# Kernel tuning notes

Measured on AMD Instinct MI355X. Metric: run time of the kernel, lower is better.

The kernel has to match this reference:

```python
import jax, jax.numpy as jnp
import numpy as np

N = 100_000      # lidar points (KITTI-scale)
E = 800_000      # knn edges, avg degree 8
C_IN = 4
INTERNAL_H, INTERNAL_W = 240, 1216   # INTERNAL_IMG_SIZE


def setup_inputs() -> dict:
    key = jax.random.key(0)
    ks = jax.random.split(key, 16)
    x = jax.random.normal(ks[0], (N, C_IN), jnp.float32)
    # lidar-like points in velodyne frame: x fwd [5,70], y left [-20,20], z up [-2,1]
    u = jax.random.uniform(ks[1], (N, 3), jnp.float32)
    pos = jnp.stack([5.0 + 65.0 * u[:, 0],
                     -20.0 + 40.0 * u[:, 1],
                     -2.0 + 3.0 * u[:, 2]], axis=1)
    edge_index = jax.random.randint(ks[2], (2, E), 0, N, dtype=jnp.int32)
    batch = jnp.zeros((N,), jnp.int32)
    # folded calibration P2 @ R0 @ Tr: pinhole cam looking down velodyne +x
    f, cx, cy = 720.0, 621.0, 250.0
    proj = jnp.array([[cx, -f, 0.0, 0.0],
                      [cy, 0.0, -f, 0.0],
                      [1.0, 0.0, 0.0, 0.0]], jnp.float32)
    dims = [(C_IN + 3, 64), (64 + 3, 128), (128 + 3, 256)]
    params = {}
    ki = 3
    for li, (din, dout) in enumerate(dims, 1):
        s1, s2 = 1.0 / np.sqrt(din), 1.0 / np.sqrt(dout)
        params[f"w1_{li}"] = jax.random.uniform(ks[ki], (din, dout), jnp.float32, -s1, s1); ki += 1
        params[f"b1_{li}"] = jnp.zeros((dout,), jnp.float32)
        params[f"w2_{li}"] = jax.random.uniform(ks[ki], (dout, dout), jnp.float32, -s2, s2); ki += 1
        params[f"b2_{li}"] = jnp.zeros((dout,), jnp.float32)
    return dict(x=x, pos=pos, edge_index=edge_index, batch=batch, proj=proj,
                img_h=375, img_w=1242, **params)


def _pointnet_conv(x, pos, src, dst, w1, b1, w2, b2):
    # message: local_nn([x_j, pos_j - pos_i]) with MLP = lin1 -> relu -> lin2; aggr = max
    m = jnp.concatenate([x[src], pos[src] - pos[dst]], axis=1)     # [E', din]
    h = jnp.maximum(m @ w1 + b1, 0.0) @ w2 + b2                    # [E', dout]
    return jax.ops.segment_max(h, dst, num_segments=x.shape[0])


def reference(x, pos, edge_index, batch, proj, img_h, img_w,
              w1_1, b1_1, w2_1, b2_1,
              w1_2, b1_2, w2_2, b2_2,
              w1_3, b1_3, w2_3, b2_3):
    n = x.shape[0]
    # PointNetConv adds self-loops by default -> every segment non-empty
    loops = jnp.arange(n, dtype=edge_index.dtype)
    src = jnp.concatenate([edge_index[0], loops])
    dst = jnp.concatenate([edge_index[1], loops])

    h = _pointnet_conv(x, pos, src, dst, w1_1, b1_1, w2_1, b2_1)   # [N, 64]
    h = _pointnet_conv(h, pos, src, dst, w1_2, b1_2, w2_2, b2_2)   # [N, 128]
    h = _pointnet_conv(h, pos, src, dst, w1_3, b1_3, w2_3, b2_3)   # [N, 256]

    # projection: (proj @ [pos; 1]) -> [3, N]; perspective divide; int16 trunc
    hom = proj @ jnp.concatenate([pos.T, jnp.ones((1, n), pos.dtype)], axis=0)
    off_u, off_v = img_w - INTERNAL_W, img_h - INTERNAL_H
    ui = (hom[0] / hom[2]).astype(jnp.int16).astype(jnp.int32) - off_u
    vi = (hom[1] / hom[2]).astype(jnp.int16).astype(jnp.int32) - off_v
    valid = (ui >= 0) & (vi >= 0) & (ui < INTERNAL_W) & (vi < INTERNAL_H)
    # route invalid points out-of-bounds so mode='drop' discards them
    ui = jnp.where(valid, ui, INTERNAL_W)
    vi = jnp.where(valid, vi, INTERNAL_H)

    img = jnp.zeros((1, h.shape[1], INTERNAL_W, INTERNAL_H), h.dtype)  # (B=1, C, 1216, 240)
    img = img.at[0, :, ui, vi].add(h, mode='drop')

    # max_pool2d(kernel=4, stride=4) -> (1, 256, 304, 60)
    B, C, W, H = img.shape
    pooled = img.reshape(B, C, W // 4, 4, H // 4, 4).max(axis=(3, 5))
    return pooled
```

## Files before the change

kernel.cpp:

```cpp
#include <hip/hip_runtime.h>
#include <cstdint>

#define N_PTS 100000
#define N_EDGE 800000
#define N_ITEMS (N_EDGE + N_PTS)
#define IMG_W 1216
#define IMG_H 240
#define OW 304
#define OH 60
#define CHUNK 32
#define BIN_BLOCKS 391

typedef _Float16 f16;
typedef _Float16 f16x8 __attribute__((ext_vector_type(8)));
typedef float f32x4 __attribute__((ext_vector_type(4)));

__device__ __forceinline__ void atomicMaxF(float* addr, float v) {
    if (v >= 0.0f) atomicMax((int*)addr, __float_as_int(v));
    else atomicMin((unsigned int*)addr, __float_as_uint(v));
}

__global__ __launch_bounds__(256)
void init_out_kernel(float* __restrict__ p, long n)
{
    long i = ((long)blockIdx.x * 256 + threadIdx.x) * 4;
    if (i < n) {
        float4 v = {-INFINITY, -INFINITY, -INFINITY, -INFINITY};
        *(float4*)&p[i] = v;
    }
}

template<int DX, int KP, int D>
__global__ __launch_bounds__(256)
void node_mfma_kernel(const float* __restrict__ X, const float* __restrict__ pos,
                      const f16* __restrict__ w1t, const float* __restrict__ b1,
                      f16* __restrict__ A)
{
    constexpr int KB = KP / 32;
    constexpr int NB = D / 16;
    const int tid = threadIdx.x;
    const int wave = tid >> 6;
    const int lane = tid & 63;
    const int row = lane & 15;
    const int kg = lane >> 4;
    const int wbase = (blockIdx.x * 4 + wave) * 32;

    f16x8 pa[2][KB];
#pragma unroll
    for (int mh = 0; mh < 2; ++mh) {
        int n = wbase + mh * 16 + row;
        int ns = (n < N_PTS) ? n : 0;
#pragma unroll
        for (int kb = 0; kb < KB; ++kb) {
            const int c0 = kb * 32 + kg * 8;
            f16x8 h;
#pragma unroll
            for (int j = 0; j < 8; ++j) {
                int k = c0 + j;
                float v = 0.0f;
                if (k < DX) v = X[(long)ns * DX + k];
                else if (k < DX + 3) v = pos[(long)ns * 3 + (k - DX)];
                h[j] = (f16)v;
            }
            pa[mh][kb] = h;
        }
    }

#pragma unroll 2
    for (int nb = 0; nb < NB; ++nb) {
        f32x4 acc0 = {0.0f, 0.0f, 0.0f, 0.0f};
        f32x4 acc1 = {0.0f, 0.0f, 0.0f, 0.0f};
#pragma unroll
        for (int kb = 0; kb < KB; ++kb) {
            f16x8 pb = *(const f16x8*)&w1t[(long)(nb * 16 + row) * KP + kb * 32 + kg * 8];
            acc0 = __builtin_amdgcn_mfma_f32_16x16x32_f16(pa[0][kb], pb, acc0, 0, 0, 0);
            acc1 = __builtin_amdgcn_mfma_f32_16x16x32_f16(pa[1][kb], pb, acc1, 0, 0, 0);
        }
        const int col = nb * 16 + row;
        const float bb = b1[col];
#pragma unroll
        for (int reg = 0; reg < 4; ++reg) {
            int r = kg * 4 + reg;
            int n0 = wbase + r;
            int n1 = wbase + 16 + r;
            if (n0 < N_PTS) A[(long)n0 * D + col] = (f16)(acc0[reg] + bb);
            if (n1 < N_PTS) A[(long)n1 * D + col] = (f16)(acc1[reg] + bb);
        }
    }
}

__global__ void cvt_w1(const float* __restrict__ w1, f16* __restrict__ w1t,
                       int K, int KP, int D)
{
    int i = blockIdx.x * 256 + threadIdx.x;
    if (i >= D * KP) return;
    int c = i / KP, k = i % KP;
    w1t[i] = (k < K) ? (f16)w1[k * D + c] : (f16)0.0f;
}

__global__ void cvt_w2(const float* __restrict__ w2, f16* __restrict__ w2t, int D)
{
    int i = blockIdx.x * 256 + threadIdx.x;
    if (i >= D * D) return;
    int n = i / D, k = i % D;
    w2t[i] = (f16)w2[k * D + n];
}

__global__ void init_hist_kernel(int* __restrict__ hist)
{
    int i = blockIdx.x * 256 + threadIdx.x;
    if (i < N_PTS) hist[i] = 1;
}

__global__ void hist_kernel(const int* __restrict__ ei, int* __restrict__ hist)
{
    int e = blockIdx.x * 256 + threadIdx.x;
    if (e < N_EDGE) atomicAdd(&hist[ei[N_EDGE + e]], 1);
}

__global__ void bsum_kernel(const int* __restrict__ hist, int* __restrict__ bsum)
{
    __shared__ int s[256];
    int i = blockIdx.x * 256 + threadIdx.x;
    s[threadIdx.x] = (i < N_PTS) ? hist[i] : 0;
    __syncthreads();
    for (int off = 128; off > 0; off >>= 1) {
        if (threadIdx.x < off) s[threadIdx.x] += s[threadIdx.x + off];
        __syncthreads();
    }
    if (threadIdx.x == 0) bsum[blockIdx.x] = s[0];
}

__global__ void scan_bsum_kernel(int* __restrict__ bsum)
{
    __shared__ int s[512];
    int t = threadIdx.x;
    int v = (t < BIN_BLOCKS) ? bsum[t] : 0;
    s[t] = v;
    __syncthreads();
    for (int off = 1; off < 512; off <<= 1) {
        int u = (t >= off) ? s[t - off] : 0;
        __syncthreads();
        s[t] += u;
        __syncthreads();
    }
    if (t < BIN_BLOCKS) bsum[t] = s[t] - v;
}

__global__ void rowptr_kernel(const int* __restrict__ hist, const int* __restrict__ bsum,
                              int* __restrict__ woff)
{
    __shared__ int s[256];
    int i = blockIdx.x * 256 + threadIdx.x;
    int v = (i < N_PTS) ? hist[i] : 0;
    s[threadIdx.x] = v;
    __syncthreads();
    for (int off = 1; off < 256; off <<= 1) {
        int u = (threadIdx.x >= off) ? s[threadIdx.x - off] : 0;
        __syncthreads();
        s[threadIdx.x] += u;
        __syncthreads();
    }
    if (i < N_PTS) woff[i] = bsum[blockIdx.x] + s[threadIdx.x] - v;
}

__global__ void scatter_edges_kernel(const int* __restrict__ ei, int* __restrict__ woff,
                                     int* __restrict__ srcS, int* __restrict__ dstS)
{
    int e = blockIdx.x * 256 + threadIdx.x;
    if (e >= N_ITEMS) return;
    int s, d;
    if (e < N_EDGE) { s = ei[e]; d = ei[N_EDGE + e]; }
    else            { s = d = e - N_EDGE; }
    int p = atomicAdd(&woff[d], 1);
    srcS[p] = s;
    dstS[p] = d;
}

template<int D>
__global__ __launch_bounds__(64)
void gemm_msg_kernel(const int* __restrict__ srcA, const int* __restrict__ dstA,
                     const f16* __restrict__ A, const float* __restrict__ pos,
                     const float* __restrict__ w1p, const f16* __restrict__ w2t,
                     const float* __restrict__ b2, float* __restrict__ OUT, int nItems)
{
    constexpr int KB = D / 32;
    constexpr int NB = D / 16;
    const int lane = threadIdx.x & 63;
    const int row = lane & 15;
    const int kg = lane >> 4;
    const long wbase = (long)blockIdx.x * 32;

    int s[2], d[2];
    float px[2], py[2], pz[2];
#pragma unroll
    for (int mh = 0; mh < 2; ++mh) {
        long e = wbase + mh * 16 + row;
        bool ok = (e < nItems);
        int ss = ok ? srcA[e] : 0;
        int dd = ok ? dstA[e] : -1;
        s[mh] = ss; d[mh] = dd;
        int dsafe = ok ? dd : 0;
        px[mh] = pos[(long)dsafe * 3 + 0];
        py[mh] = pos[(long)dsafe * 3 + 1];
        pz[mh] = pos[(long)dsafe * 3 + 2];
    }

    f16x8 pa[2][KB];
#pragma unroll
    for (int kb = 0; kb < KB; ++kb) {
        const int c0 = kb * 32 + kg * 8;
        f16x8 a0 = *(const f16x8*)&A[(long)s[0] * D + c0];
        f16x8 a1 = *(const f16x8*)&A[(long)s[1] * D + c0];
        f16x8 h0, h1;
#pragma unroll
        for (int j = 0; j < 8; ++j) {
            float wx = w1p[c0 + j];
            float wy = w1p[D + c0 + j];
            float wz = w1p[2 * D + c0 + j];
            h0[j] = (f16)fmaxf((float)a0[j] - (px[0] * wx + py[0] * wy + pz[0] * wz), 0.0f);
            h1[j] = (f16)fmaxf((float)a1[j] - (px[1] * wx + py[1] * wy + pz[1] * wz), 0.0f);
        }
        pa[0][kb] = h0;
        pa[1][kb] = h1;
    }

    int dd0[4], dd1[4];
#pragma unroll
    for (int reg = 0; reg < 4; ++reg) {
        int r = kg * 4 + reg;
        dd0[reg] = __shfl(d[0], r);
        dd1[reg] = __shfl(d[1], r);
    }
    const bool a01 = (dd0[1] == dd0[0]), a12 = (dd0[2] == dd0[1]), a23 = (dd0[3] == dd0[2]);
    const bool b01 = (dd1[1] == dd1[0]), b12 = (dd1[2] == dd1[1]), b23 = (dd1[3] == dd1[2]);
    const bool aAll = a01 && a12 && a23, bAll = b01 && b12 && b23;
    const int aN0 = __shfl(dd0[0], lane + 16);
    const int bN0 = __shfl(dd1[0], lane + 16);
    const int aFn = __shfl((int)aAll, lane + 16);
    const int bFn = __shfl((int)bAll, lane + 16);
    const bool aCo = (kg < 3) && (dd0[3] == aN0);
    const bool bCo = (kg < 3) && (dd1[3] == bN0);
    const int lprev = (lane >= 16) ? (lane - 16) : 0;
    const int aP3 = __shfl(dd0[3], lprev);
    const int bP3 = __shfl(dd1[3], lprev);
    const bool aHd = (kg == 0) || (dd0[0] != aP3);
    const bool bHd = (kg == 0) || (dd1[0] != bP3);

#pragma unroll
    for (int nb = 0; nb < NB; ++nb) {
        f32x4 acc0 = {0.0f, 0.0f, 0.0f, 0.0f};
        f32x4 acc1 = {0.0f, 0.0f, 0.0f, 0.0f};
#pragma unroll
        for (int kb = 0; kb < KB; ++kb) {
            f16x8 pb = *(const f16x8*)&w2t[(long)(nb * 16 + row) * D + kb * 32 + kg * 8];
            acc0 = __builtin_amdgcn_mfma_f32_16x16x32_f16(pa[0][kb], pb, acc0, 0, 0, 0);
            acc1 = __builtin_amdgcn_mfma_f32_16x16x32_f16(pa[1][kb], pb, acc1, 0, 0, 0);
        }
        const int col = nb * 16 + row;
        const float bb = b2[col];
        {
            const float v0 = acc0[0] + bb, v1 = acc0[1] + bb, v2 = acc0[2] + bb, v3 = acc0[3] + bb;
            const float s3 = v3;
            const float s2 = a23 ? fmaxf(v2, s3) : v2;
            const float s1 = a12 ? fmaxf(v1, s2) : v1;
            const float s0 = a01 ? fmaxf(v0, s1) : v0;
            float P = v0;
            P = a01 ? fmaxf(P, v1) : P;
            P = (a01 && a12) ? fmaxf(P, v2) : P;
            P = aAll ? fmaxf(P, v3) : P;
            float T = -INFINITY;
#pragma unroll
            for (int it = 0; it < 3; ++it) {
                float Pn = __shfl(P, lane + 16);
                float Tn = __shfl(T, lane + 16);
                T = aCo ? fmaxf(Pn, aFn ? Tn : -INFINITY) : T;
            }
            const float x0 = aAll ? fmaxf(s0, T) : s0;
            const float x1 = (a12 && a23) ? fmaxf(s1, T) : s1;
            const float x2 = a23 ? fmaxf(s2, T) : s2;
            const float x3 = fmaxf(s3, T);
            if (aHd  && dd0[0] >= 0) atomicMaxF(&OUT[(long)dd0[0] * D + col], x0);
            if (!a01 && dd0[1] >= 0) atomicMaxF(&OUT[(long)dd0[1] * D + col], x1);
            if (!a12 && dd0[2] >= 0) atomicMaxF(&OUT[(long)dd0[2] * D + col], x2);
            if (!a23 && dd0[3] >= 0) atomicMaxF(&OUT[(long)dd0[3] * D + col], x3);
        }
        {
            const float v0 = acc1[0] + bb, v1 = acc1[1] + bb, v2 = acc1[2] + bb, v3 = acc1[3] + bb;
            const float s3 = v3;
            const float s2 = b23 ? fmaxf(v2, s3) : v2;
            const float s1 = b12 ? fmaxf(v1, s2) : v1;
            const float s0 = b01 ? fmaxf(v0, s1) : v0;
            float P = v0;
            P = b01 ? fmaxf(P, v1) : P;
            P = (b01 && b12) ? fmaxf(P, v2) : P;
            P = bAll ? fmaxf(P, v3) : P;
            float T = -INFINITY;
#pragma unroll
            for (int it = 0; it < 3; ++it) {
                float Pn = __shfl(P, lane + 16);
                float Tn = __shfl(T, lane + 16);
                T = bCo ? fmaxf(Pn, bFn ? Tn : -INFINITY) : T;
            }
            const float x0 = bAll ? fmaxf(s0, T) : s0;
            const float x1 = (b12 && b23) ? fmaxf(s1, T) : s1;
            const float x2 = b23 ? fmaxf(s2, T) : s2;
            const float x3 = fmaxf(s3, T);
            if (bHd  && dd1[0] >= 0) atomicMaxF(&OUT[(long)dd1[0] * D + col], x0);
            if (!b01 && dd1[1] >= 0) atomicMaxF(&OUT[(long)dd1[1] * D + col], x1);
            if (!b12 && dd1[2] >= 0) atomicMaxF(&OUT[(long)dd1[2] * D + col], x2);
            if (!b23 && dd1[3] >= 0) atomicMaxF(&OUT[(long)dd1[3] * D + col], x3);
        }
    }
}

__global__ __launch_bounds__(64)
void gemm_msg256_kernel(const int* __restrict__ srcA, const int* __restrict__ dstA,
                        const f16* __restrict__ A, const float* __restrict__ pos,
                        const float* __restrict__ w1p, const f16* __restrict__ w2t,
                        const float* __restrict__ b2, float* __restrict__ OUT, int nItems)
{
    const int lane = threadIdx.x & 63;
    const int row = lane & 15;
    const int kg = lane >> 4;
    const long wbase = (long)blockIdx.x * 32;

    int s[2], d[2];
    float px[2], py[2], pz[2];
#pragma unroll
    for (int mh = 0; mh < 2; ++mh) {
        long e = wbase + mh * 16 + row;
        bool ok = (e < nItems);
        int ss = ok ? srcA[e] : 0;
        int dd = ok ? dstA[e] : -1;
        s[mh] = ss; d[mh] = dd;
        int dsafe = ok ? dd : 0;
        px[mh] = pos[(long)dsafe * 3 + 0];
        py[mh] = pos[(long)dsafe * 3 + 1];
        pz[mh] = pos[(long)dsafe * 3 + 2];
    }

    f16x8 pa[2][8];
#pragma unroll
    for (int kb = 0; kb < 8; ++kb) {
        const int c0 = kb * 32 + kg * 8;
        f16x8 a0 = *(const f16x8*)&A[(long)s[0] * 256 + c0];
        f16x8 a1 = *(const f16x8*)&A[(long)s[1] * 256 + c0];
        f16x8 h0, h1;
#pragma unroll
        for (int j = 0; j < 8; ++j) {
            float wx = w1p[c0 + j];
            float wy = w1p[256 + c0 + j];
            float wz = w1p[512 + c0 + j];
            h0[j] = (f16)fmaxf((float)a0[j] - (px[0] * wx + py[0] * wy + pz[0] * wz), 0.0f);
            h1[j] = (f16)fmaxf((float)a1[j] - (px[1] * wx + py[1] * wy + pz[1] * wz), 0.0f);
        }
        pa[0][kb] = h0;
        pa[1][kb] = h1;
    }

    int dd0[4], dd1[4];
#pragma unroll
    for (int reg = 0; reg < 4; ++reg) {
        int r = kg * 4 + reg;
        dd0[reg] = __shfl(d[0], r);
        dd1[reg] = __shfl(d[1], r);
    }
    bool hd0[4], hd1[4];
    hd0[0] = true; hd1[0] = true;
#pragma unroll
    for (int reg = 1; reg < 4; ++reg) {
        hd0[reg] = (dd0[reg] != dd0[reg - 1]);
        hd1[reg] = (dd1[reg] != dd1[reg - 1]);
    }

#pragma unroll
    for (int nb = 0; nb < 16; ++nb) {
        f32x4 acc0 = {0.0f, 0.0f, 0.0f, 0.0f};
        f32x4 acc1 = {0.0f, 0.0f, 0.0f, 0.0f};
#pragma unroll
        for (int kb = 0; kb < 8; ++kb) {
            f16x8 pb = *(const f16x8*)&w2t[(long)(nb * 16 + row) * 256 + kb * 32 + kg * 8];
            acc0 = __builtin_amdgcn_mfma_f32_16x16x32_f16(pa[0][kb], pb, acc0, 0, 0, 0);
            acc1 = __builtin_amdgcn_mfma_f32_16x16x32_f16(pa[1][kb], pb, acc1, 0, 0, 0);
        }
        const int col = nb * 16 + row;
        const float bb = b2[col];
        float v0[4], v1[4];
#pragma unroll
        for (int reg = 0; reg < 4; ++reg) { v0[reg] = acc0[reg] + bb; v1[reg] = acc1[reg] + bb; }
        float s0[4], s1[4];
        s0[3] = v0[3]; s1[3] = v1[3];
#pragma unroll
        for (int reg = 2; reg >= 0; --reg) {
            s0[reg] = hd0[reg + 1] ? v0[reg] : fmaxf(v0[reg], s0[reg + 1]);
            s1[reg] = hd1[reg + 1] ? v1[reg] : fmaxf(v1[reg], s1[reg + 1]);
        }
#pragma unroll
        for (int reg = 0; reg < 4; ++reg) {
            if (hd0[reg] && dd0[reg] >= 0) atomicMaxF(&OUT[(long)dd0[reg] * 256 + col], s0[reg]);
            if (hd1[reg] && dd1[reg] >= 0) atomicMaxF(&OUT[(long)dd1[reg] * 256 + col], s1[reg]);
        }
    }
}

__global__ void proj_kernel(const float* __restrict__ pos, const float* __restrict__ proj,
                            const int* __restrict__ img_h, const int* __restrict__ img_w,
                            int* __restrict__ pix)
{
    int n = blockIdx.x * blockDim.x + threadIdx.x;
    if (n >= N_PTS) return;
    float px = pos[n * 3 + 0], py = pos[n * 3 + 1], pz = pos[n * 3 + 2];
    float h0 = proj[0] * px + proj[1] * py + proj[2]  * pz + proj[3];
    float h1 = proj[4] * px + proj[5] * py + proj[6]  * pz + proj[7];
    float h2 = proj[8] * px + proj[9] * py + proj[10] * pz + proj[11];
    int off_u = img_w[0] - IMG_W;
    int off_v = img_h[0] - IMG_H;
    int ui = (int)(short)(h0 / h2) - off_u;
    int vi = (int)(short)(h1 / h2) - off_v;
    bool valid = (ui >= 0) && (vi >= 0) && (ui < IMG_W) && (vi < IMG_H);
    pix[n] = valid ? (ui * IMG_H + vi) : -1;
}

__global__ __launch_bounds__(256)
void scatter_kernel(const float* __restrict__ H, const int* __restrict__ pix,
                    float* __restrict__ img, int cbase)
{
    long g = (long)blockIdx.x * blockDim.x + threadIdx.x;
    if (g >= (long)N_PTS * CHUNK) return;
    int n = (int)(g / CHUNK);
    int c = (int)(g % CHUNK);
    int p = pix[n];
    if (p < 0) return;
    atomicAdd(&img[(long)p * CHUNK + c], H[(long)n * 256 + cbase + c]);
}

__global__ __launch_bounds__(CHUNK)
void pool_kernel(const float* __restrict__ img, float* __restrict__ out, int cbase)
{
    int cell = blockIdx.x;
    int wc = cell / OH, hc = cell % OH;
    int c = threadIdx.x;
    float mx = -INFINITY;
#pragma unroll
    for (int i = 0; i < 4; ++i)
#pragma unroll
        for (int j = 0; j < 4; ++j) {
            long p = (long)(wc * 4 + i) * IMG_H + (hc * 4 + j);
            mx = fmaxf(mx, img[p * CHUNK + c]);
        }
    out[(long)(cbase + c) * (OW * OH) + wc * OH + hc] = mx;
}

extern "C" void kernel_launch(void* const* d_in, const int* in_sizes, int n_in,
                              void* d_out, int out_size, void* d_ws, size_t ws_size,
                              hipStream_t stream)
{
    const float* x     = (const float*)d_in[0];
    const float* pos   = (const float*)d_in[1];
    const int*   ei    = (const int*)d_in[2];
    const float* proj  = (const float*)d_in[4];
    const int*   img_h = (const int*)d_in[5];
    const int*   img_w = (const int*)d_in[6];
    const float* w1_1 = (const float*)d_in[7];
    const float* b1_1 = (const float*)d_in[8];
    const float* w2_1 = (const float*)d_in[9];
    const float* b2_1 = (const float*)d_in[10];
    const float* w1_2 = (const float*)d_in[11];
    const float* b1_2 = (const float*)d_in[12];
    const float* w2_2 = (const float*)d_in[13];
    const float* b2_2 = (const float*)d_in[14];
    const float* w1_3 = (const float*)d_in[15];
    const float* b1_3 = (const float*)d_in[16];
    const float* w2_3 = (const float*)d_in[17];
    const float* b2_3 = (const float*)d_in[18];
    float* out = (float*)d_out;

    if (ws_size < 162400000ull) return;
    char* ws = (char*)d_ws;
    float* HH   = (float*)(ws + 0);
    float* F1   = (float*)(ws + 0);
    float* F0   = (float*)(ws + 51200000);
    f16*   A12  = (f16*)(ws + 76800000);
    f16*   A3   = (f16*)(ws + 102400000);
    float* img  = (float*)(ws + 102400000);
    int*   pix  = (int*)(ws + 153600000);
    f16*   w2t3 = (f16*)(ws + 154000000);
    f16*   w2t2 = (f16*)(ws + 154131072);
    f16*   w2t1 = (f16*)(ws + 154163840);
    int*   srcS = (int*)(ws + 154200000);
    int*   dstS = (int*)(ws + 157800000);
    int*   hist = (int*)(ws + 161400000);
    int*   woff = (int*)(ws + 161800000);
    int*   bsum = (int*)(ws + 162200000);
    f16*   w1t3 = (f16*)(ws + 162210000);
    f16*   w1t2 = (f16*)(ws + 162300000);
    f16*   w1t1 = (f16*)(ws + 162330000);

    const int NODE_BLOCKS = (N_PTS + 127) / 128;
    const int WIN_BLOCKS  = (N_ITEMS + 31) / 32;
    const int E256  = (N_EDGE + 255) / 256;
    const int I256  = (N_ITEMS + 255) / 256;

    init_hist_kernel<<<BIN_BLOCKS, 256, 0, stream>>>(hist);
    hist_kernel<<<E256, 256, 0, stream>>>(ei, hist);
    bsum_kernel<<<BIN_BLOCKS, 256, 0, stream>>>(hist, bsum);
    scan_bsum_kernel<<<1, 512, 0, stream>>>(bsum);
    rowptr_kernel<<<BIN_BLOCKS, 256, 0, stream>>>(hist, bsum, woff);
    scatter_edges_kernel<<<I256, 256, 0, stream>>>(ei, woff, srcS, dstS);

    cvt_w1<<<(64 * 32 + 255) / 256, 256, 0, stream>>>(w1_1, w1t1, 7, 32, 64);
    cvt_w1<<<(128 * 96 + 255) / 256, 256, 0, stream>>>(w1_2, w1t2, 67, 96, 128);
    cvt_w1<<<(256 * 160 + 255) / 256, 256, 0, stream>>>(w1_3, w1t3, 131, 160, 256);
    cvt_w2<<<(64 * 64 + 255) / 256, 256, 0, stream>>>(w2_1, w2t1, 64);
    cvt_w2<<<(128 * 128 + 255) / 256, 256, 0, stream>>>(w2_2, w2t2, 128);
    cvt_w2<<<(256 * 256 + 255) / 256, 256, 0, stream>>>(w2_3, w2t3, 256);
    proj_kernel<<<(N_PTS + 255) / 256, 256, 0, stream>>>(pos, proj, img_h, img_w, pix);
    init_out_kernel<<<(N_PTS * 64 / 4 + 255) / 256, 256, 0, stream>>>(F0, (long)N_PTS * 64);
    init_out_kernel<<<(N_PTS * 128 / 4 + 255) / 256, 256, 0, stream>>>(F1, (long)N_PTS * 128);

    node_mfma_kernel<4, 32, 64><<<NODE_BLOCKS, 256, 0, stream>>>(x, pos, w1t1, b1_1, A12);
    gemm_msg_kernel<64><<<WIN_BLOCKS, 64, 0, stream>>>(srcS, dstS, A12, pos, w1_1 + 4 * 64, w2t1, b2_1, F0, N_ITEMS);

    node_mfma_kernel<64, 96, 128><<<NODE_BLOCKS, 256, 0, stream>>>(F0, pos, w1t2, b1_2, A12);
    gemm_msg_kernel<128><<<WIN_BLOCKS, 64, 0, stream>>>(srcS, dstS, A12, pos, w1_2 + 64 * 128, w2t2, b2_2, F1, N_ITEMS);

    node_mfma_kernel<128, 160, 256><<<NODE_BLOCKS, 256, 0, stream>>>(F1, pos, w1t3, b1_3, A3);
    init_out_kernel<<<(N_PTS * 256 / 4 + 255) / 256, 256, 0, stream>>>(HH, (long)N_PTS * 256);
    gemm_msg256_kernel<<<WIN_BLOCKS, 64, 0, stream>>>(srcS, dstS, A3, pos, w1_3 + 128 * 256, w2t3, b2_3, HH, N_ITEMS);

    for (int cb = 0; cb < 256; cb += CHUNK) {
        hipMemsetAsync(img, 0, (size_t)IMG_W * IMG_H * CHUNK * 4, stream);
        scatter_kernel<<<(N_PTS * CHUNK) / 256, 256, 0, stream>>>(HH, pix, img, cb);
        pool_kernel<<<OW * OH, CHUNK, 0, stream>>>(img, out, cb);
    }
}
```

Baseline: 1.573 ms.

## Store per-node conv outputs channel-major and transpose via shared memory in scatter

Switches the layout of the max-aggregated outputs (F0, F1, HH) from node-major [N, D] to channel-major [D, N]. Atomic max writes from each MFMA column then target one contiguous channel row, so lanes in the same column that hit nearby sorted destinations land closer together. The node kernels read the transposed input, and the image scatter now stages a 32-channel by 64-node tile in shared memory before issuing atomicAdd. The cost is that node_mfma reads of X become strided by N_PTS per channel, which is less coalesced for the gather.

```diff
diff --git a/kernel.cpp b/kernel.cpp
--- a/kernel.cpp
+++ b/kernel.cpp
@@ -30,7 +30,7 @@
     }
 }
 
-template<int DX, int KP, int D>
+template<int DX, int KP, int D, bool XT>
 __global__ __launch_bounds__(256)
 void node_mfma_kernel(const float* __restrict__ X, const float* __restrict__ pos,
                       const f16* __restrict__ w1t, const float* __restrict__ b1,
@@ -58,7 +58,7 @@
             for (int j = 0; j < 8; ++j) {
                 int k = c0 + j;
                 float v = 0.0f;
-                if (k < DX) v = X[(long)ns * DX + k];
+                if (k < DX) v = XT ? X[(long)k * N_PTS + ns] : X[(long)ns * DX + k];
                 else if (k < DX + 3) v = pos[(long)ns * 3 + (k - DX)];
                 h[j] = (f16)v;
             }
@@ -258,6 +258,7 @@
             acc1 = __builtin_amdgcn_mfma_f32_16x16x32_f16(pa[1][kb], pb, acc1, 0, 0, 0);
         }
         const int col = nb * 16 + row;
+        float* outc = OUT + (long)col * N_PTS;
         const float bb = b2[col];
         {
             const float v0 = acc0[0] + bb, v1 = acc0[1] + bb, v2 = acc0[2] + bb, v3 = acc0[3] + bb;
@@ -280,10 +281,10 @@
             const float x1 = (a12 && a23) ? fmaxf(s1, T) : s1;
             const float x2 = a23 ? fmaxf(s2, T) : s2;
             const float x3 = fmaxf(s3, T);
-            if (aHd  && dd0[0] >= 0) atomicMaxF(&OUT[(long)dd0[0] * D + col], x0);
-            if (!a01 && dd0[1] >= 0) atomicMaxF(&OUT[(long)dd0[1] * D + col], x1);
-            if (!a12 && dd0[2] >= 0) atomicMaxF(&OUT[(long)dd0[2] * D + col], x2);
-            if (!a23 && dd0[3] >= 0) atomicMaxF(&OUT[(long)dd0[3] * D + col], x3);
+            if (aHd  && dd0[0] >= 0) atomicMaxF(&outc[dd0[0]], x0);
+            if (!a01 && dd0[1] >= 0) atomicMaxF(&outc[dd0[1]], x1);
+            if (!a12 && dd0[2] >= 0) atomicMaxF(&outc[dd0[2]], x2);
+            if (!a23 && dd0[3] >= 0) atomicMaxF(&outc[dd0[3]], x3);
         }
         {
             const float v0 = acc1[0] + bb, v1 = acc1[1] + bb, v2 = acc1[2] + bb, v3 = acc1[3] + bb;
@@ -306,10 +307,10 @@
             const float x1 = (b12 && b23) ? fmaxf(s1, T) : s1;
             const float x2 = b23 ? fmaxf(s2, T) : s2;
             const float x3 = fmaxf(s3, T);
-            if (bHd  && dd1[0] >= 0) atomicMaxF(&OUT[(long)dd1[0] * D + col], x0);
-            if (!b01 && dd1[1] >= 0) atomicMaxF(&OUT[(long)dd1[1] * D + col], x1);
-            if (!b12 && dd1[2] >= 0) atomicMaxF(&OUT[(long)dd1[2] * D + col], x2);
-            if (!b23 && dd1[3] >= 0) atomicMaxF(&OUT[(long)dd1[3] * D + col], x3);
+            if (bHd  && dd1[0] >= 0) atomicMaxF(&outc[dd1[0]], x0);
+            if (!b01 && dd1[1] >= 0) atomicMaxF(&outc[dd1[1]], x1);
+            if (!b12 && dd1[2] >= 0) atomicMaxF(&outc[dd1[2]], x2);
+            if (!b23 && dd1[3] >= 0) atomicMaxF(&outc[dd1[3]], x3);
         }
     }
 }
@@ -385,6 +386,7 @@
             acc1 = __builtin_amdgcn_mfma_f32_16x16x32_f16(pa[1][kb], pb, acc1, 0, 0, 0);
         }
         const int col = nb * 16 + row;
+        float* outc = OUT + (long)col * N_PTS;
         const float bb = b2[col];
         float v0[4], v1[4];
 #pragma unroll
@@ -398,8 +400,8 @@
         }
 #pragma unroll
         for (int reg = 0; reg < 4; ++reg) {
-            if (hd0[reg] && dd0[reg] >= 0) atomicMaxF(&OUT[(long)dd0[reg] * 256 + col], s0[reg]);
-            if (hd1[reg] && dd1[reg] >= 0) atomicMaxF(&OUT[(long)dd1[reg] * 256 + col], s1[reg]);
+            if (hd0[reg] && dd0[reg] >= 0) atomicMaxF(&outc[dd0[reg]], s0[reg]);
+            if (hd1[reg] && dd1[reg] >= 0) atomicMaxF(&outc[dd1[reg]], s1[reg]);
         }
     }
 }
@@ -423,16 +425,28 @@
 }
 
 __global__ __launch_bounds__(256)
-void scatter_kernel(const float* __restrict__ H, const int* __restrict__ pix,
-                    float* __restrict__ img, int cbase)
-{
-    long g = (long)blockIdx.x * blockDim.x + threadIdx.x;
-    if (g >= (long)N_PTS * CHUNK) return;
-    int n = (int)(g / CHUNK);
-    int c = (int)(g % CHUNK);
-    int p = pix[n];
-    if (p < 0) return;
-    atomicAdd(&img[(long)p * CHUNK + c], H[(long)n * 256 + cbase + c]);
+void scatter_t_kernel(const float* __restrict__ H, const int* __restrict__ pix,
+                      float* __restrict__ img, int cbase)
+{
+    __shared__ float tile[CHUNK][65];
+    __shared__ int ptile[64];
+    const int nb0 = blockIdx.x * 64;
+    const int t = threadIdx.x;
+    for (int i = t; i < CHUNK * 64; i += 256) {
+        int c = i >> 6, nl = i & 63;
+        int n = nb0 + nl;
+        tile[c][nl] = (n < N_PTS) ? H[(long)(cbase + c) * N_PTS + n] : 0.0f;
+    }
+    if (t < 64) {
+        int n = nb0 + t;
+        ptile[t] = (n < N_PTS) ? pix[n] : -1;
+    }
+    __syncthreads();
+    for (int i = t; i < CHUNK * 64; i += 256) {
+        int c = i & 31, nl = i >> 5;
+        int p = ptile[nl];
+        if (p >= 0) atomicAdd(&img[(long)p * CHUNK + c], tile[c][nl]);
+    }
 }
 
 __global__ __launch_bounds__(CHUNK)
@@ -501,6 +515,7 @@
     const int WIN_BLOCKS  = (N_ITEMS + 31) / 32;
     const int E256  = (N_EDGE + 255) / 256;
     const int I256  = (N_ITEMS + 255) / 256;
+    const int SC_BLOCKS = (N_PTS + 63) / 64;
 
     init_hist_kernel<<<BIN_BLOCKS, 256, 0, stream>>>(hist);
     hist_kernel<<<E256, 256, 0, stream>>>(ei, hist);
@@ -519,19 +534,19 @@
     init_out_kernel<<<(N_PTS * 64 / 4 + 255) / 256, 256, 0, stream>>>(F0, (long)N_PTS * 64);
     init_out_kernel<<<(N_PTS * 128 / 4 + 255) / 256, 256, 0, stream>>>(F1, (long)N_PTS * 128);
 
-    node_mfma_kernel<4, 32, 64><<<NODE_BLOCKS, 256, 0, stream>>>(x, pos, w1t1, b1_1, A12);
+    node_mfma_kernel<4, 32, 64, false><<<NODE_BLOCKS, 256, 0, stream>>>(x, pos, w1t1, b1_1, A12);
     gemm_msg_kernel<64><<<WIN_BLOCKS, 64, 0, stream>>>(srcS, dstS, A12, pos, w1_1 + 4 * 64, w2t1, b2_1, F0, N_ITEMS);
 
-    node_mfma_kernel<64, 96, 128><<<NODE_BLOCKS, 256, 0, stream>>>(F0, pos, w1t2, b1_2, A12);
+    node_mfma_kernel<64, 96, 128, true><<<NODE_BLOCKS, 256, 0, stream>>>(F0, pos, w1t2, b1_2, A12);
     gemm_msg_kernel<128><<<WIN_BLOCKS, 64, 0, stream>>>(srcS, dstS, A12, pos, w1_2 + 64 * 128, w2t2, b2_2, F1, N_ITEMS);
 
-    node_mfma_kernel<128, 160, 256><<<NODE_BLOCKS, 256, 0, stream>>>(F1, pos, w1t3, b1_3, A3);
+    node_mfma_kernel<128, 160, 256, true><<<NODE_BLOCKS, 256, 0, stream>>>(F1, pos, w1t3, b1_3, A3);
     init_out_kernel<<<(N_PTS * 256 / 4 + 255) / 256, 256, 0, stream>>>(HH, (long)N_PTS * 256);
     gemm_msg256_kernel<<<WIN_BLOCKS, 64, 0, stream>>>(srcS, dstS, A3, pos, w1_3 + 128 * 256, w2t3, b2_3, HH, N_ITEMS);
 
     for (int cb = 0; cb < 256; cb += CHUNK) {
         hipMemsetAsync(img, 0, (size_t)IMG_W * IMG_H * CHUNK * 4, stream);
-        scatter_kernel<<<(N_PTS * CHUNK) / 256, 256, 0, stream>>>(HH, pix, img, cb);
+        scatter_t_kernel<<<SC_BLOCKS, 256, 0, stream>>>(HH, pix, img, cb);
         pool_kernel<<<OW * OH, CHUNK, 0, stream>>>(img, out, cb);
     }
 }
```

After: 3.833 ms. +143.7%, slower.

## Replace chunked atomic image scatter with pixel-sorted CSR gather pooling

Applied to the files above, without the earlier changes.

Replaces the eight-pass loop that zeroed a dense image chunk, atomically scattered point features and max-pooled it with a counting sort of points by pixel (histogram, scan, scatter) and a single pooling kernel. The new kernel gathers and sums each pixel's point features before taking the max. This drops eight large memsets, the float atomics and the dense image traffic. In exchange it adds several small sort kernels, including a single-block carry scan, and the gather reads from HH are irregular.

```diff
diff --git a/kernel.cpp b/kernel.cpp
--- a/kernel.cpp
+++ b/kernel.cpp
@@ -8,8 +8,10 @@
 #define IMG_H 240
 #define OW 304
 #define OH 60
-#define CHUNK 32
+#define N_PIX (IMG_W * IMG_H)
+#define N_BIN (N_PIX + 1)
 #define BIN_BLOCKS 391
+#define BIN2_BLOCKS ((N_BIN + 255) / 256)
 
 typedef _Float16 f16;
 typedef _Float16 f16x8 __attribute__((ext_vector_type(8)));
@@ -422,34 +424,97 @@
     pix[n] = valid ? (ui * IMG_H + vi) : -1;
 }
 
+__global__ void hist2_kernel(const int* __restrict__ pix, int* __restrict__ hist2)
+{
+    int n = blockIdx.x * 256 + threadIdx.x;
+    if (n < N_PTS) atomicAdd(&hist2[pix[n] + 1], 1);
+}
+
+__global__ void bsum2_kernel(const int* __restrict__ h, int* __restrict__ bs)
+{
+    __shared__ int s[256];
+    int i = blockIdx.x * 256 + threadIdx.x;
+    s[threadIdx.x] = (i < N_BIN) ? h[i] : 0;
+    __syncthreads();
+    for (int off = 128; off > 0; off >>= 1) {
+        if (threadIdx.x < off) s[threadIdx.x] += s[threadIdx.x + off];
+        __syncthreads();
+    }
+    if (threadIdx.x == 0) bs[blockIdx.x] = s[0];
+}
+
+__global__ void scan_carry_kernel(int* __restrict__ bs, int nb)
+{
+    __shared__ int s[256];
+    __shared__ int carry;
+    if (threadIdx.x == 0) carry = 0;
+    __syncthreads();
+    for (int base = 0; base < nb; base += 256) {
+        int i = base + threadIdx.x;
+        int v = (i < nb) ? bs[i] : 0;
+        s[threadIdx.x] = v;
+        __syncthreads();
+        for (int off = 1; off < 256; off <<= 1) {
+            int u = (threadIdx.x >= off) ? s[threadIdx.x - off] : 0;
+            __syncthreads();
+            s[threadIdx.x] += u;
+            __syncthreads();
+        }
+        if (i < nb) bs[i] = carry + s[threadIdx.x] - v;
+        __syncthreads();
+        if (threadIdx.x == 255) carry += s[255];
+        __syncthreads();
+    }
+}
+
+__global__ void rowptr2_kernel(const int* __restrict__ h, const int* __restrict__ bs,
+                               int* __restrict__ woff2)
+{
+    __shared__ int s[256];
+    int i = blockIdx.x * 256 + threadIdx.x;
+    int v = (i < N_BIN) ? h[i] : 0;
+    s[threadIdx.x] = v;
+    __syncthreads();
+    for (int off = 1; off < 256; off <<= 1) {
+        int u = (threadIdx.x >= off) ? s[threadIdx.x - off] : 0;
+        __syncthreads();
+        s[threadIdx.x] += u;
+        __syncthreads();
+    }
+    if (i < N_BIN) woff2[i] = bs[blockIdx.x] + s[threadIdx.x] - v;
+}
+
+__global__ void scatter_points_kernel(const int* __restrict__ pix, int* __restrict__ woff2,
+                                      int* __restrict__ psort)
+{
+    int n = blockIdx.x * 256 + threadIdx.x;
+    if (n >= N_PTS) return;
+    int p = atomicAdd(&woff2[pix[n] + 1], 1);
+    psort[p] = n;
+}
+
 __global__ __launch_bounds__(256)
-void scatter_kernel(const float* __restrict__ H, const int* __restrict__ pix,
-                    float* __restrict__ img, int cbase)
-{
-    long g = (long)blockIdx.x * blockDim.x + threadIdx.x;
-    if (g >= (long)N_PTS * CHUNK) return;
-    int n = (int)(g / CHUNK);
-    int c = (int)(g % CHUNK);
-    int p = pix[n];
-    if (p < 0) return;
-    atomicAdd(&img[(long)p * CHUNK + c], H[(long)n * 256 + cbase + c]);
-}
-
-__global__ __launch_bounds__(CHUNK)
-void pool_kernel(const float* __restrict__ img, float* __restrict__ out, int cbase)
-{
-    int cell = blockIdx.x;
-    int wc = cell / OH, hc = cell % OH;
-    int c = threadIdx.x;
+void pool2_kernel(const float* __restrict__ HH, const int* __restrict__ psort,
+                  const int* __restrict__ wend, float* __restrict__ out)
+{
+    const int cell = blockIdx.x;
+    const int wc = cell / OH, hc = cell % OH;
+    const int c = threadIdx.x;
     float mx = -INFINITY;
 #pragma unroll
-    for (int i = 0; i < 4; ++i)
+    for (int i = 0; i < 4; ++i) {
 #pragma unroll
         for (int j = 0; j < 4; ++j) {
-            long p = (long)(wc * 4 + i) * IMG_H + (hc * 4 + j);
-            mx = fmaxf(mx, img[p * CHUNK + c]);
-        }
-    out[(long)(cbase + c) * (OW * OH) + wc * OH + hc] = mx;
+            int b = (wc * 4 + i) * IMG_H + (hc * 4 + j) + 1;
+            int st = wend[b - 1];
+            int en = wend[b];
+            float sum = 0.0f;
+            for (int p = st; p < en; ++p)
+                sum += HH[(long)psort[p] * 256 + c];
+            mx = fmaxf(mx, sum);
+        }
+    }
+    out[(long)c * (OW * OH) + cell] = mx;
 }
 
 extern "C" void kernel_launch(void* const* d_in, const int* in_sizes, int n_in,
@@ -483,7 +548,10 @@
     float* F0   = (float*)(ws + 51200000);
     f16*   A12  = (f16*)(ws + 76800000);
     f16*   A3   = (f16*)(ws + 102400000);
-    float* img  = (float*)(ws + 102400000);
+    int*   hist2 = (int*)(ws + 102400000);
+    int*   woff2 = (int*)(ws + 103700000);
+    int*   bsum2 = (int*)(ws + 105000000);
+    int*   psort = (int*)(ws + 105100000);
     int*   pix  = (int*)(ws + 153600000);
     f16*   w2t3 = (f16*)(ws + 154000000);
     f16*   w2t2 = (f16*)(ws + 154131072);
@@ -501,6 +569,7 @@
     const int WIN_BLOCKS  = (N_ITEMS + 31) / 32;
     const int E256  = (N_EDGE + 255) / 256;
     const int I256  = (N_ITEMS + 255) / 256;
+    const int P256  = (N_PTS + 255) / 256;
 
     init_hist_kernel<<<BIN_BLOCKS, 256, 0, stream>>>(hist);
     hist_kernel<<<E256, 256, 0, stream>>>(ei, hist);
@@ -515,7 +584,7 @@
     cvt_w2<<<(64 * 64 + 255) / 256, 256, 0, stream>>>(w2_1, w2t1, 64);
     cvt_w2<<<(128 * 128 + 255) / 256, 256, 0, stream>>>(w2_2, w2t2, 128);
     cvt_w2<<<(256 * 256 + 255) / 256, 256, 0, stream>>>(w2_3, w2t3, 256);
-    proj_kernel<<<(N_PTS + 255) / 256, 256, 0, stream>>>(pos, proj, img_h, img_w, pix);
+    proj_kernel<<<P256, 256, 0, stream>>>(pos, proj, img_h, img_w, pix);
     init_out_kernel<<<(N_PTS * 64 / 4 + 255) / 256, 256, 0, stream>>>(F0, (long)N_PTS * 64);
     init_out_kernel<<<(N_PTS * 128 / 4 + 255) / 256, 256, 0, stream>>>(F1, (long)N_PTS * 128);
 
@@ -529,9 +598,11 @@
     init_out_kernel<<<(N_PTS * 256 / 4 + 255) / 256, 256, 0, stream>>>(HH, (long)N_PTS * 256);
     gemm_msg256_kernel<<<WIN_BLOCKS, 64, 0, stream>>>(srcS, dstS, A3, pos, w1_3 + 128 * 256, w2t3, b2_3, HH, N_ITEMS);
 
-    for (int cb = 0; cb < 256; cb += CHUNK) {
-        hipMemsetAsync(img, 0, (size_t)IMG_W * IMG_H * CHUNK * 4, stream);
-        scatter_kernel<<<(N_PTS * CHUNK) / 256, 256, 0, stream>>>(HH, pix, img, cb);
-        pool_kernel<<<OW * OH, CHUNK, 0, stream>>>(img, out, cb);
-    }
-}
+    hipMemsetAsync(hist2, 0, N_BIN * 4, stream);
+    hist2_kernel<<<P256, 256, 0, stream>>>(pix, hist2);
+    bsum2_kernel<<<BIN2_BLOCKS, 256, 0, stream>>>(hist2, bsum2);
+    scan_carry_kernel<<<1, 256, 0, stream>>>(bsum2, BIN2_BLOCKS);
+    rowptr2_kernel<<<BIN2_BLOCKS, 256, 0, stream>>>(hist2, bsum2, woff2);
+    scatter_points_kernel<<<P256, 256, 0, stream>>>(pix, woff2, psort);
+    pool2_kernel<<<OW * OH, 256, 0, stream>>>(HH, psort, woff2, out);
+}
```

Result: slower. 1.649 ms (+4.8%).
